# Performance work log

Measured on AMD Instinct MI355X. Metric: run time of the kernel, lower is better.

The kernel has to match this reference:

```python
import jax, jax.numpy as jnp
import numpy as np

DIM, N_HEADS, HEAD_DIM, BASE = 1024, 16, 64, 10000.0
B, S = 2, 2048


def setup_inputs() -> dict:
    key = jax.random.key(0)
    ks = jax.random.split(key, 8)
    theta = (BASE ** (-jnp.arange(0, HEAD_DIM, 2, dtype=jnp.float32) / HEAD_DIM))  # [head_dim//2]
    s = 0.02
    return {
        "x": jax.random.normal(ks[0], (B, S, DIM), jnp.float32),
        "positions": jnp.arange(S, dtype=jnp.int32),
        "theta": theta,
        "Wq": jax.random.normal(ks[1], (DIM, N_HEADS * HEAD_DIM), jnp.float32) * s,
        "bq": jnp.zeros((N_HEADS * HEAD_DIM,), jnp.float32),
        "Wk": jax.random.normal(ks[2], (DIM, N_HEADS * HEAD_DIM), jnp.float32) * s,
        "bk": jnp.zeros((N_HEADS * HEAD_DIM,), jnp.float32),
        "Wv": jax.random.normal(ks[3], (DIM, N_HEADS * HEAD_DIM), jnp.float32) * s,
        "bv": jnp.zeros((N_HEADS * HEAD_DIM,), jnp.float32),
        "Wo": jax.random.normal(ks[4], (N_HEADS * HEAD_DIM, DIM), jnp.float32) * s,
        "bo": jnp.zeros((DIM,), jnp.float32),
    }


def _rope(x, theta):
    # x: [B, H, S, head_dim]; theta: [head_dim//2]
    seq_len = x.shape[2]
    ang = jnp.arange(seq_len, dtype=x.dtype)[:, None] * theta  # [S, head_dim//2]
    cos = jnp.cos(ang)[None, None]  # [1,1,S,head_dim//2]
    sin = jnp.sin(ang)[None, None]
    x1, x2 = x[..., 0::2], x[..., 1::2]
    # matches torch.cat([-x2*sin + x1*cos, x1*sin + x2*cos], dim=-1)
    return jnp.concatenate([x1 * cos - x2 * sin, x1 * sin + x2 * cos], axis=-1)


def reference(x, positions, theta, Wq, bq, Wk, bk, Wv, bv, Wo, bo):
    batch, seq_len, _ = x.shape
    H, hd = N_HEADS, HEAD_DIM

    def split_heads(t):
        return t.reshape(batch, seq_len, H, hd).transpose(0, 2, 1, 3)  # [B,H,S,hd]

    q = split_heads(x @ Wq + bq)
    k = split_heads(x @ Wk + bk)
    v = split_heads(x @ Wv + bv)
    q = _rope(q, theta)
    k = _rope(k, theta)

    scale = 1.0 / jnp.sqrt(jnp.asarray(hd, x.dtype))
    scores = jnp.einsum("bhqd,bhkd->bhqk", q, k) * scale  # [B,H,S,S]
    causal = jnp.tril(jnp.ones((seq_len, seq_len), dtype=bool))
    scores = jnp.where(causal, scores, jnp.asarray(-jnp.inf, x.dtype))
    attn = jax.nn.softmax(scores, axis=-1)  # dropout is identity at eval
    out = jnp.einsum("bhqk,bhkd->bhqd", attn, v)  # [B,H,S,hd]
    out = out.transpose(0, 2, 1, 3).reshape(batch, seq_len, H * hd)
    return out @ Wo + bo
```

## Files before the change

kernel.cpp:

```cpp
#include <hip/hip_runtime.h>
#include <math.h>

#define B_   2
#define S_   2048
#define DIM_ 1024
#define H_   16
#define HD_  64
#define BS_  (B_ * S_)
#define BHSD ((size_t)B_ * H_ * S_ * HD_)
#define CEXP 0.1803368801111244f

typedef unsigned short u16;
typedef unsigned int   u32;
typedef short s16x8 __attribute__((ext_vector_type(8)));
typedef float f32x4 __attribute__((ext_vector_type(4)));

#define MFMA16(a, b, c) __builtin_amdgcn_mfma_f32_16x16x32_bf16((a), (b), (c), 0, 0, 0)

__device__ __forceinline__ u16 f2bf(float f) {
    u32 u = __float_as_uint(f);
    u += 0x7fffu + ((u >> 16) & 1u);
    return (u16)(u >> 16);
}
__device__ __forceinline__ u32 cvt_pk_bf16(float a, float b) {
    u32 r;
    asm("v_cvt_pk_bf16_f32 %0, %1, %2" : "=v"(r) : "v"(a), "v"(b));
    return r;
}
__device__ __forceinline__ void gl16(void* lds, const void* g) {
    __builtin_amdgcn_global_load_lds(
        (__attribute__((address_space(1))) void*)(g),
        (__attribute__((address_space(3))) void*)(lds), 16, 0, 0);
}

__global__ __launch_bounds__(256) void prep(
    const float* __restrict__ x, u16* __restrict__ xb,
    const float* __restrict__ W0, const float* __restrict__ W1,
    const float* __restrict__ W2, const float* __restrict__ W3,
    u16* __restrict__ T0, u16* __restrict__ T1,
    u16* __restrict__ T2, u16* __restrict__ T3,
    const float* __restrict__ bq, const float* __restrict__ bk,
    const float* __restrict__ bv, float* __restrict__ bias3,
    const float* __restrict__ theta, float2* __restrict__ cs)
{
    __shared__ float tile[32][33];
    const int bid = blockIdx.x, tid = threadIdx.x;

    if (bid < 2048) {
        const int i = bid * 256 + tid;
        const float4 a = *(const float4*)(x + (size_t)i * 8);
        const float4 b = *(const float4*)(x + (size_t)i * 8 + 4);
        s16x8 o;
        o[0] = (short)f2bf(a.x); o[1] = (short)f2bf(a.y);
        o[2] = (short)f2bf(a.z); o[3] = (short)f2bf(a.w);
        o[4] = (short)f2bf(b.x); o[5] = (short)f2bf(b.y);
        o[6] = (short)f2bf(b.z); o[7] = (short)f2bf(b.w);
        *(s16x8*)(xb + (size_t)i * 8) = o;
    } else if (bid < 6144) {
        const int idx = bid - 2048;
        const int z = idx >> 10;
        const float* W; u16* T;
        switch (z) {
            case 0: W = W0; T = T0; break;
            case 1: W = W1; T = T1; break;
            case 2: W = W2; T = T2; break;
            default: W = W3; T = T3; break;
        }
        const int n0 = ((idx >> 5) & 31) * 32, k0 = (idx & 31) * 32;
        const int c = tid & 31, rr = tid >> 5;
#pragma unroll
        for (int i = 0; i < 4; ++i) {
            const int k = rr + i * 8;
            tile[k][c] = W[(size_t)(k0 + k) * DIM_ + n0 + c];
        }
        __syncthreads();
#pragma unroll
        for (int i = 0; i < 4; ++i) {
            const int col = n0 + rr + i * 8;
            int pcol = col;
            if (z < 2) {
                const int dd = col & 63;
                const int pd = (dd & 1) ? 32 + (dd >> 1) : (dd >> 1);
                pcol = (col & ~63) | pd;
            }
            T[(size_t)pcol * DIM_ + k0 + c] = f2bf(tile[c][rr + i * 8]);
        }
    } else if (bid < 6400) {
        const int idx = bid - 6144;
        const int s = idx * 8 + (tid >> 5), j = tid & 31;
        float sn, cn;
        sincosf((float)s * theta[j], &sn, &cn);
        cs[(s << 5) + j] = make_float2(cn, sn);
    } else {
        const int i = (bid - 6400) * 256 + tid;
        const int which = i >> 10, local = i & 1023;
        const float v = (which == 0) ? bq[local]
                      : (which == 1) ? bk[local] : bv[local];
        int dst = i;
        if (which < 2) {
            const int dd = local & 63;
            const int pd = (dd & 1) ? 32 + (dd >> 1) : (dd >> 1);
            dst = which * 1024 + (local & ~63) + pd;
        }
        bias3[dst] = v;
    }
}

template<int BN, int HMIN, int EPI>
__global__ __launch_bounds__(256, 3) void gemm_mfma(
    const u16* __restrict__ A, const u16* __restrict__ Bt,
    const float* __restrict__ bias, void* __restrict__ Yv,
    const float2* __restrict__ cs)
{
    __shared__ u16 As[128 * 64];
    __shared__ u16 Bs[BN * 64];

    const int tid = threadIdx.x, lane = tid & 63, wid = tid >> 6;
    const int l15 = lane & 15, lg = lane >> 4;
    const int row0 = blockIdx.x * 128, col0 = blockIdx.y * BN;
    const int wr = (wid >> 1) * 64;
    const int wc = (wid & 1) * (BN / 2);
    constexpr int NM = 4, NN = BN / 32, BCH = BN / 32;

    const int l8 = lane >> 3, l7 = lane & 7;
    const int colE = ((l7 ^ l8) << 3);

    const u16* aptr[4]; u16* aldp[4];
#pragma unroll
    for (int i = 0; i < 4; ++i) {
        const int ci = wid * 4 + i;
        const int rr = row0 + ci * 8 + l8;
        size_t a0;
        if (HMIN)
            a0 = (((size_t)(rr >> 11) * H_) * S_ + (rr & (S_ - 1))) * HD_ + colE;
        else
            a0 = (size_t)rr * DIM_ + colE;
        aptr[i] = A + a0;
        aldp[i] = As + ci * 512;
    }
    const u16* bptr[BCH]; u16* bldp[BCH];
#pragma unroll
    for (int i = 0; i < BCH; ++i) {
        const int ci = wid * BCH + i;
        const int rr = col0 + ci * 8 + l8;
        bptr[i] = Bt + (size_t)rr * DIM_ + colE;
        bldp[i] = Bs + ci * 512;
    }
    const size_t astep = HMIN ? (size_t)S_ * HD_ : 64;

    f32x4 acc[NM][NN];
#pragma unroll
    for (int m = 0; m < NM; ++m)
#pragma unroll
        for (int n = 0; n < NN; ++n) acc[m][n] = (f32x4){0.f, 0.f, 0.f, 0.f};

    for (int k0 = 0; k0 < DIM_; k0 += 64) {
        __syncthreads();
#pragma unroll
        for (int i = 0; i < 4; ++i) gl16(aldp[i], aptr[i]);
#pragma unroll
        for (int i = 0; i < BCH; ++i) gl16(bldp[i], bptr[i]);
#pragma unroll
        for (int i = 0; i < 4; ++i) aptr[i] += astep;
#pragma unroll
        for (int i = 0; i < BCH; ++i) bptr[i] += 64;
        __syncthreads();

        s16x8 af[NM][2], bfr[NN][2];
#pragma unroll
        for (int m = 0; m < NM; ++m) {
            const int row = wr + m * 16 + l15;
#pragma unroll
            for (int kf = 0; kf < 2; ++kf)
                af[m][kf] = *(const s16x8*)&As[row * 64 +
                    (((kf * 64 + lg * 16) ^ ((l15 & 7) << 4)) >> 1)];
        }
#pragma unroll
        for (int n = 0; n < NN; ++n) {
            const int row = wc + n * 16 + l15;
#pragma unroll
            for (int kf = 0; kf < 2; ++kf)
                bfr[n][kf] = *(const s16x8*)&Bs[row * 64 +
                    (((kf * 64 + lg * 16) ^ ((l15 & 7) << 4)) >> 1)];
        }
        __builtin_amdgcn_s_setprio(1);
#pragma unroll
        for (int m = 0; m < NM; ++m)
#pragma unroll
            for (int n = 0; n < NN; ++n) {
                acc[m][n] = MFMA16(af[m][0], bfr[n][0], acc[m][n]);
                acc[m][n] = MFMA16(af[m][1], bfr[n][1], acc[m][n]);
            }
        __builtin_amdgcn_s_setprio(0);
    }

    if (EPI == 0) {
        u16* Y = (u16*)Yv;
        const int whichq = (col0 + wc) >> 10;
        if (whichq < 2) {
            const float sclw = (whichq == 0) ? CEXP : 1.0f;
#pragma unroll
            for (int n = 0; n < 2; ++n) {
                const int cc0 = col0 + wc + n * 16 + l15;
                const int j = n * 16 + l15;
                const float bv0 = bias[cc0];
                const float bv1 = bias[cc0 + 32];
                const int hh = (cc0 >> 6) & (H_ - 1);
#pragma unroll
                for (int m = 0; m < NM; ++m)
#pragma unroll
                    for (int r = 0; r < 4; ++r) {
                        const int rr = row0 + wr + m * 16 + lg * 4 + r;
                        const int b = rr >> 11, s = rr & (S_ - 1);
                        const float2 csv = cs[(s << 5) + j];
                        const float v0 = acc[m][n][r] + bv0;
                        const float v1 = acc[m][n + 2][r] + bv1;
                        const size_t base = (size_t)whichq * BHSD
                            + (((size_t)b * H_ + hh) * S_ + s) * HD_;
                        Y[base + j]      = f2bf((v0 * csv.x - v1 * csv.y) * sclw);
                        Y[base + j + 32] = f2bf((v0 * csv.y + v1 * csv.x) * sclw);
                    }
            }
        } else {
#pragma unroll
            for (int n = 0; n < NN; ++n) {
                const int cc = col0 + wc + n * 16 + l15;
                const float bv = bias[cc];
                const int hh = (cc >> 6) & (H_ - 1), d = cc & 63;
#pragma unroll
                for (int m = 0; m < NM; ++m)
#pragma unroll
                    for (int r = 0; r < 4; ++r) {
                        const int rr = row0 + wr + m * 16 + lg * 4 + r;
                        const int b = rr >> 11, s = rr & (S_ - 1);
                        const int sp = (s & ~60) | ((s & 12) << 1)
                                     | ((s & 16) << 1) | ((s & 32) >> 3);
                        Y[2 * BHSD + ((size_t)(b * H_ + hh) * HD_ + d) * S_ + sp] =
                            f2bf(acc[m][n][r] + bv);
                    }
            }
        }
    } else {
#pragma unroll
        for (int n = 0; n < NN; ++n) {
            const int cc = col0 + wc + n * 16 + l15;
            const float bv = bias[cc];
#pragma unroll
            for (int m = 0; m < NM; ++m)
#pragma unroll
                for (int r = 0; r < 4; ++r) {
                    const int rr = row0 + wr + m * 16 + lg * 4 + r;
                    ((float*)Yv)[(size_t)rr * DIM_ + cc] = acc[m][n][r] + bv;
                }
        }
    }
}

__global__ __launch_bounds__(256, 4) void attn_q(
    u16* __restrict__ Q, const u16* __restrict__ K, const u16* __restrict__ VT)
{
    const int bh = blockIdx.x;
    const int qt = 31 - blockIdx.y;
    const int nsteps = qt + 1;

    u16* Qg = Q + (size_t)bh * S_ * HD_;
    const u16* Kg = K + (size_t)bh * S_ * HD_;
    const u16* Vg = VT + (size_t)bh * HD_ * S_;

    __shared__ u16 Ks[2][64 * 64];
    __shared__ u16 Vs[2][64 * 64];

    const int tid = threadIdx.x;
    const int w = tid >> 6, lane = tid & 63;
    const int q0 = qt * 64 + w * 16;
    const int l15 = lane & 15, lg = lane >> 4;

    const int crow = lane >> 3, cslt = lane & 7;

    auto stage = [&](int bufi, int j0) {
#pragma unroll
        for (int i = 0; i < 2; ++i) {
            const int c = w * 2 + i;
            const int row = c * 8 + crow;
            const int soff = ((cslt ^ (row & 7)) << 3);
            gl16(&Ks[bufi][c * 512], Kg + (size_t)(j0 + row) * HD_ + soff);
            gl16(&Vs[bufi][c * 512], Vg + (size_t)row * S_ + j0 + soff);
        }
    };

    s16x8 qf[2];
    {
        const u16* qrow = Qg + (size_t)(q0 + l15) * HD_ + lg * 8;
        qf[0] = *(const s16x8*)(qrow);
        qf[1] = *(const s16x8*)(qrow + 32);
    }

    s16x8 onesv;
#pragma unroll
    for (int i = 0; i < 8; ++i) onesv[i] = (short)0x3F80;

    f32x4 o[4], ol;
#pragma unroll
    for (int n = 0; n < 4; ++n) o[n] = (f32x4){0.f, 0.f, 0.f, 0.f};
    ol = (f32x4){0.f, 0.f, 0.f, 0.f};

    stage(0, 0);
    __syncthreads();

    int buf = 0;
    for (int t = 0; t < nsteps; ++t) {
        if (t + 1 < nsteps) stage(buf ^ 1, (t + 1) * 64);

        const u16* Kb = Ks[buf];
        const u16* Vb = Vs[buf];

        f32x4 sc[4];
        __builtin_amdgcn_s_setprio(1);
#pragma unroll
        for (int sub = 0; sub < 4; ++sub) {
            const int kr = sub * 16 + l15;
            const s16x8 kf0 = *(const s16x8*)&Kb[kr * 64 + ((lg ^ (kr & 7)) << 3)];
            const s16x8 kf1 = *(const s16x8*)&Kb[kr * 64 + (((lg + 4) ^ (kr & 7)) << 3)];
            f32x4 z = (f32x4){0.f, 0.f, 0.f, 0.f};
            z = MFMA16(kf0, qf[0], z);
            sc[sub] = MFMA16(kf1, qf[1], z);
        }
        __builtin_amdgcn_s_setprio(0);

        if (t == qt) {
#pragma unroll
            for (int sub = 0; sub < 4; ++sub) {
                if (sub == w) {
#pragma unroll
                    for (int r = 0; r < 4; ++r)
                        if (lg * 4 + r > l15) sc[sub][r] = -1e30f;
                } else if (sub > w) {
#pragma unroll
                    for (int r = 0; r < 4; ++r) sc[sub][r] = -1e30f;
                }
            }
        }

        float p[4][4];
#pragma unroll
        for (int sub = 0; sub < 4; ++sub)
#pragma unroll
            for (int r = 0; r < 4; ++r)
                p[sub][r] = __builtin_amdgcn_exp2f(sc[sub][r]);

        union { s16x8 v; u32 w4[4]; } af[2];
#pragma unroll
        for (int step = 0; step < 2; ++step)
#pragma unroll
            for (int jj = 0; jj < 4; ++jj) {
                const int sub = (jj >> 1) * 2 + step;
                const int r0  = (jj & 1) * 2;
                af[step].w4[jj] = cvt_pk_bf16(p[sub][r0], p[sub][r0 + 1]);
            }
        __builtin_amdgcn_s_setprio(1);
#pragma unroll
        for (int n = 0; n < 4; ++n) {
            const int d = n * 16 + l15;
            const s16x8 vf0 = *(const s16x8*)&Vb[d * 64 + ((lg ^ (d & 7)) << 3)];
            const s16x8 vf1 = *(const s16x8*)&Vb[d * 64 + (((lg + 4) ^ (d & 7)) << 3)];
            o[n] = MFMA16(af[0].v, vf0, o[n]);
            o[n] = MFMA16(af[1].v, vf1, o[n]);
        }
        ol = MFMA16(af[0].v, onesv, ol);
        ol = MFMA16(af[1].v, onesv, ol);
        __builtin_amdgcn_s_setprio(0);

        __syncthreads();
        buf ^= 1;
    }

    f32x4 il;
#pragma unroll
    for (int r = 0; r < 4; ++r) il[r] = 1.f / ol[r];
    u16* orow = Qg + (size_t)(q0 + lg * 4) * HD_ + l15;
#pragma unroll
    for (int r = 0; r < 4; ++r)
#pragma unroll
        for (int n = 0; n < 4; ++n)
            orow[r * HD_ + n * 16] = f2bf(o[n][r] * il[r]);
}

extern "C" void kernel_launch(void* const* d_in, const int* in_sizes, int n_in,
                              void* d_out, int out_size, void* d_ws, size_t ws_size,
                              hipStream_t stream)
{
    (void)in_sizes; (void)n_in; (void)out_size; (void)ws_size;
    const float* x     = (const float*)d_in[0];
    const float* theta = (const float*)d_in[2];
    const float* Wq    = (const float*)d_in[3];
    const float* bq    = (const float*)d_in[4];
    const float* Wk    = (const float*)d_in[5];
    const float* bk    = (const float*)d_in[6];
    const float* Wv    = (const float*)d_in[7];
    const float* bv    = (const float*)d_in[8];
    const float* Wo    = (const float*)d_in[9];
    const float* bo    = (const float*)d_in[10];
    float* out = (float*)d_out;

    u16* xb  = (u16*)d_ws;
    u16* wtq = xb + (size_t)BS_ * DIM_;
    u16* wtk = wtq + (size_t)DIM_ * DIM_;
    u16* wtv = wtk + (size_t)DIM_ * DIM_;
    u16* wto = wtv + (size_t)DIM_ * DIM_;
    u16* qws = wto + (size_t)DIM_ * DIM_;
    u16* kws = qws + BHSD;
    u16* vtw = kws + BHSD;
    float* bias3 = (float*)(vtw + BHSD);
    float2* cs = (float2*)(bias3 + 4096);

    prep<<<dim3(6412), dim3(256), 0, stream>>>(
        x, xb, Wq, Wk, Wv, Wo, wtq, wtk, wtv, wto, bq, bk, bv, bias3, theta, cs);

    gemm_mfma<128, 0, 0><<<dim3(32, 24), dim3(256), 0, stream>>>(
        xb, wtq, bias3, qws, cs);

    attn_q<<<dim3(32, 32), dim3(256), 0, stream>>>(qws, kws, vtw);

    gemm_mfma<64, 1, 1><<<dim3(32, 16), dim3(256), 0, stream>>>(
        qws, wto, bo, out, cs);
}
```

Measured before the change: 91.18 us.

## Split causal attention KV range in two halves and merge partials

Each query tile's KV loop is split into two halves handled by separate blocks (split-K / flash-decoding style). Block ordering interleaves long and short tiles to balance load, and occupancy is raised to 5 blocks per CU. A new merge kernel adds the bf16 partial outputs and row sums, then normalizes. This aims to fix the load imbalance of the causal triangle, at the cost of an extra launch, workspace traffic, and bf16 rounding of unnormalized partials. The softmax has no running max, so partial sums combine by plain addition.

```diff
diff --git a/kernel.cpp b/kernel.cpp
--- a/kernel.cpp
+++ b/kernel.cpp
@@ -21,6 +21,9 @@
     u32 u = __float_as_uint(f);
     u += 0x7fffu + ((u >> 16) & 1u);
     return (u16)(u >> 16);
+}
+__device__ __forceinline__ float bf2f(u16 h) {
+    return __uint_as_float(((u32)h) << 16);
 }
 __device__ __forceinline__ u32 cvt_pk_bf16(float a, float b) {
     u32 r;
@@ -256,14 +259,23 @@
     }
 }
 
-__global__ __launch_bounds__(256, 4) void attn_q(
-    u16* __restrict__ Q, const u16* __restrict__ K, const u16* __restrict__ VT)
+__global__ __launch_bounds__(256, 5) void attn_q(
+    const u16* __restrict__ Q, const u16* __restrict__ K,
+    const u16* __restrict__ VT, u16* __restrict__ Opart,
+    float* __restrict__ lpart)
 {
     const int bh = blockIdx.x;
-    const int qt = 31 - blockIdx.y;
-    const int nsteps = qt + 1;
-
-    u16* Qg = Q + (size_t)bh * S_ * HD_;
+    const int y  = blockIdx.y;
+    const int a = y >> 4, r0_ = y & 15;
+    const int b = r0_ >> 1, half = r0_ & 1;
+    const int qt = (a == 0) ? (31 - b) : (a == 1) ? (16 + b)
+                 : (a == 2) ? (15 - b) : b;
+    const int T = qt + 1, h0 = (T + 1) >> 1;
+    const int kvlo = half ? h0 : 0;
+    const int kvhi = half ? T : h0;
+    const int nst = kvhi - kvlo;
+
+    const u16* Qg = Q + (size_t)bh * S_ * HD_;
     const u16* Kg = K + (size_t)bh * S_ * HD_;
     const u16* Vg = VT + (size_t)bh * HD_ * S_;
 
@@ -304,12 +316,13 @@
     for (int n = 0; n < 4; ++n) o[n] = (f32x4){0.f, 0.f, 0.f, 0.f};
     ol = (f32x4){0.f, 0.f, 0.f, 0.f};
 
-    stage(0, 0);
+    stage(0, kvlo * 64);
     __syncthreads();
 
     int buf = 0;
-    for (int t = 0; t < nsteps; ++t) {
-        if (t + 1 < nsteps) stage(buf ^ 1, (t + 1) * 64);
+    for (int s = 0; s < nst; ++s) {
+        const int t = kvlo + s;
+        if (s + 1 < nst) stage(buf ^ 1, (t + 1) * 64);
 
         const u16* Kb = Ks[buf];
         const u16* Vb = Vs[buf];
@@ -354,8 +367,8 @@
 #pragma unroll
             for (int jj = 0; jj < 4; ++jj) {
                 const int sub = (jj >> 1) * 2 + step;
-                const int r0  = (jj & 1) * 2;
-                af[step].w4[jj] = cvt_pk_bf16(p[sub][r0], p[sub][r0 + 1]);
+                const int rr0 = (jj & 1) * 2;
+                af[step].w4[jj] = cvt_pk_bf16(p[sub][rr0], p[sub][rr0 + 1]);
             }
         __builtin_amdgcn_s_setprio(1);
 #pragma unroll
@@ -374,15 +387,43 @@
         buf ^= 1;
     }
 
-    f32x4 il;
-#pragma unroll
-    for (int r = 0; r < 4; ++r) il[r] = 1.f / ol[r];
-    u16* orow = Qg + (size_t)(q0 + lg * 4) * HD_ + l15;
-#pragma unroll
-    for (int r = 0; r < 4; ++r)
+    const size_t it = ((size_t)(bh * 32 + qt) * 2 + half);
+    u16* op = Opart + it * 4096;
+#pragma unroll
+    for (int r = 0; r < 4; ++r) {
+        const int rowl = w * 16 + lg * 4 + r;
 #pragma unroll
         for (int n = 0; n < 4; ++n)
-            orow[r * HD_ + n * 16] = f2bf(o[n][r] * il[r]);
+            op[rowl * 64 + n * 16 + l15] = f2bf(o[n][r]);
+        if (l15 == 0) lpart[it * 64 + rowl] = ol[r];
+    }
+}
+
+__global__ __launch_bounds__(256) void attn_merge(
+    const u16* __restrict__ Opart, const float* __restrict__ lpart,
+    u16* __restrict__ Q)
+{
+    const int bh = blockIdx.x, qt = blockIdx.y, tid = threadIdx.x;
+    const size_t it0 = (size_t)(bh * 32 + qt) * 2;
+    const int row = tid >> 2, c0 = (tid & 3) * 16;
+
+    const float l = lpart[it0 * 64 + row] + lpart[(it0 + 1) * 64 + row];
+    const float inv = 1.f / l;
+
+    const u16* p0 = Opart + it0 * 4096 + row * 64 + c0;
+    const u16* p1 = p0 + 4096;
+    u16* dst = Q + ((size_t)bh * S_ + qt * 64 + row) * HD_ + c0;
+
+    const s16x8 a0 = *(const s16x8*)p0,       a1 = *(const s16x8*)p1;
+    const s16x8 b0 = *(const s16x8*)(p0 + 8), b1 = *(const s16x8*)(p1 + 8);
+    s16x8 oA, oB;
+#pragma unroll
+    for (int j = 0; j < 8; ++j) {
+        oA[j] = (short)f2bf((bf2f((u16)a0[j]) + bf2f((u16)a1[j])) * inv);
+        oB[j] = (short)f2bf((bf2f((u16)b0[j]) + bf2f((u16)b1[j])) * inv);
+    }
+    *(s16x8*)dst = oA;
+    *(s16x8*)(dst + 8) = oB;
 }
 
 extern "C" void kernel_launch(void* const* d_in, const int* in_sizes, int n_in,
@@ -412,6 +453,8 @@
     u16* vtw = kws + BHSD;
     float* bias3 = (float*)(vtw + BHSD);
     float2* cs = (float2*)(bias3 + 4096);
+    u16* opart = (u16*)(cs + (size_t)S_ * 32);
+    float* lpart = (float*)(opart + (size_t)2048 * 4096);
 
     prep<<<dim3(6412), dim3(256), 0, stream>>>(
         x, xb, Wq, Wk, Wv, Wo, wtq, wtk, wtv, wto, bq, bk, bv, bias3, theta, cs);
@@ -419,7 +462,9 @@
     gemm_mfma<128, 0, 0><<<dim3(32, 24), dim3(256), 0, stream>>>(
         xb, wtq, bias3, qws, cs);
 
-    attn_q<<<dim3(32, 32), dim3(256), 0, stream>>>(qws, kws, vtw);
+    attn_q<<<dim3(32, 64), dim3(256), 0, stream>>>(qws, kws, vtw, opart, lpart);
+
+    attn_merge<<<dim3(32, 32), dim3(256), 0, stream>>>(opart, lpart, qws);
 
     gemm_mfma<64, 1, 1><<<dim3(32, 16), dim3(256), 0, stream>>>(
         qws, wto, bo, out, cs);
```

Measured after the change: 91.93 us. Within noise of the previous version (+0.8%).
